# Kernel tuning notes

Measured on AMD Instinct MI355X. Metric: run time of the kernel, lower is better.

The kernel has to match this reference:

```python
import jax, jax.numpy as jnp
import numpy as np

HEADS = 4
DIM_HEAD = 32
EPS = 1e-5

def _layernorm(x, g, b):
    mu = jnp.mean(x, axis=-1, keepdims=True)
    var = jnp.var(x, axis=-1, keepdims=True)
    return (x - mu) * jax.lax.rsqrt(var + EPS) * g + b

def setup_inputs() -> dict:
    key = jax.random.key(0)
    ks = jax.random.split(key, 8)
    B, C, H, W = 16, 256, 32, 32
    N = H * W
    inner = HEADS * DIM_HEAD  # 128
    s = lambda d: 1.0 / np.sqrt(d)
    return {
        "x": jax.random.normal(ks[0], (B, C, H, W), jnp.float32),
        "pos_embedding": jax.random.normal(ks[1], (1, N, C), jnp.float32),
        "w_qkv": jax.random.normal(ks[2], (C, inner * 3), jnp.float32) * s(C),
        "w_out": jax.random.normal(ks[3], (inner, C), jnp.float32) * s(inner),
        "b_out": jnp.zeros((C,), jnp.float32),
        "w_ff1": jax.random.normal(ks[4], (C, inner), jnp.float32) * s(C),
        "b_ff1": jnp.zeros((inner,), jnp.float32),
        "w_ff2": jax.random.normal(ks[5], (inner, C), jnp.float32) * s(inner),
        "b_ff2": jnp.zeros((C,), jnp.float32),
        "g1": jnp.ones((C,), jnp.float32),
        "beta1": jnp.zeros((C,), jnp.float32),
        "g2": jnp.ones((C,), jnp.float32),
        "beta2": jnp.zeros((C,), jnp.float32),
    }

def reference(x, pos_embedding, w_qkv, w_out, b_out, w_ff1, b_ff1, w_ff2, b_ff2, g1, beta1, g2, beta2):
    b, c, h, w = x.shape
    n = h * w
    tok = jnp.transpose(x.reshape(b, c, n), (0, 2, 1))  # [b, n, c]
    tok = tok + pos_embedding  # (dropout is identity at eval)
    # attention
    qkv = _layernorm(tok, g1, beta1) @ w_qkv  # [b, n, 3*inner]
    qkv = qkv.reshape(b, n, 3, HEADS, DIM_HEAD)
    q, k, v = qkv[:, :, 0], qkv[:, :, 1], qkv[:, :, 2]  # [b, n, h, d]
    scale = DIM_HEAD ** -0.5
    dots = jnp.einsum('bihd,bjhd->bhij', q, k) * scale
    attn = jax.nn.softmax(dots, axis=-1)
    out = jnp.einsum('bhij,bjhd->bihd', attn, v).reshape(b, n, HEADS * DIM_HEAD)
    tok = out @ w_out + b_out + tok
    # ffn
    hdn = jax.nn.gelu(_layernorm(tok, g2, beta2) @ w_ff1 + b_ff1, approximate=False)
    tok = hdn @ w_ff2 + b_ff2 + tok
    return jnp.transpose(tok, (0, 2, 1)).reshape(b, c, h, w)
```

## Files before the change

### kernel.cpp

```cpp
#include <hip/hip_runtime.h>
#include <hip/hip_bf16.h>
#include <math.h>

#define B_     16
#define C_     256
#define N_     1024
#define HEADS_ 4
#define DH_    32
#define INNER_ 128
#define EPS_   1e-5f

typedef __attribute__((ext_vector_type(8))) short bf16x8;
typedef __attribute__((ext_vector_type(4))) float f32x4;

__device__ __forceinline__ ushort f2bf(float f) {
  union { float f; unsigned u; } v; v.f = f;
  unsigned u = v.u;
  return (ushort)((u + 0x7fffu + ((u >> 16) & 1u)) >> 16);
}
__device__ __forceinline__ float bf2f(ushort u) {
  union { unsigned u; float f; } v; v.u = ((unsigned)u) << 16;
  return v.f;
}
__device__ __forceinline__ unsigned cvt_pk_bf16(float lo, float hi) {
  unsigned r;
  asm("v_cvt_pk_bf16_f32 %0, %1, %2" : "=v"(r) : "v"(lo), "v"(hi));
  return r;
}

#define QSCALE_ 0.2550348652979437f

__global__ __launch_bounds__(256) void k_wconv(
    const float* __restrict__ wqkv, const float* __restrict__ wout,
    const float* __restrict__ wff1, const float* __restrict__ wff2,
    ushort* __restrict__ wqkvT, ushort* __restrict__ woutT,
    ushort* __restrict__ wff1T, ushort* __restrict__ wff2T) {
  int i = blockIdx.x * 256 + threadIdx.x;
  if (i < 98304) {
    int k = i / 384, n = i % 384;
    wqkvT[n * 256 + k] = f2bf(wqkv[i]);
    return;
  }
  i -= 98304;
  if (i < 32768) {
    int k = i / 256, n = i % 256;
    woutT[n * 128 + k] = f2bf(wout[i]);
    return;
  }
  i -= 32768;
  if (i < 32768) {
    int k = i / 128, n = i % 128;
    wff1T[n * 256 + k] = f2bf(wff1[i]);
    return;
  }
  i -= 32768;
  {
    int k = i / 256, n = i % 256;
    wff2T[n * 128 + k] = f2bf(wff2[i]);
  }
}

union KFusedSmem {
  float  xs[C_][68];
  ushort xnl[64][264];
};

__global__ __launch_bounds__(256) void k_fused(
    const float* __restrict__ x, const float* __restrict__ pos,
    const float* __restrict__ g1, const float* __restrict__ beta1,
    const ushort* __restrict__ wqkvT, ushort* __restrict__ tokb,
    ushort* __restrict__ qb, ushort* __restrict__ kb, ushort* __restrict__ vtb) {
  const int b  = blockIdx.x >> 4;
  const int n0 = (blockIdx.x & 15) << 6;
  const int t  = threadIdx.x;
  __shared__ KFusedSmem u;

  {
    const int cq = t >> 4, nq = t & 15;
#pragma unroll
    for (int i = 0; i < 16; ++i) {
      const int c = i * 16 + cq;
      const float4 v = *reinterpret_cast<const float4*>(
          &x[((size_t)b * C_ + c) * N_ + n0 + 4 * nq]);
      *reinterpret_cast<float4*>(&u.xs[c][4 * nq]) = v;
    }
  }
  __syncthreads();

  {
    const int tl = t >> 2, sub = t & 3, c0 = sub * 64;
    const int n = n0 + tl;
    float v[64];
#pragma unroll
    for (int i = 0; i < 64; ++i) v[i] = u.xs[c0 + i][tl];
#pragma unroll
    for (int j = 0; j < 16; ++j) {
      const float4 p = *reinterpret_cast<const float4*>(&pos[(size_t)n * C_ + c0 + 4 * j]);
      v[4*j] += p.x; v[4*j+1] += p.y; v[4*j+2] += p.z; v[4*j+3] += p.w;
    }
    float s = 0.f;
#pragma unroll
    for (int i = 0; i < 64; ++i) s += v[i];
    s += __shfl_xor(s, 1); s += __shfl_xor(s, 2);
    const float mu = s * (1.f / C_);
    float sq = 0.f;
#pragma unroll
    for (int i = 0; i < 64; ++i) { const float d = v[i] - mu; sq += d * d; }
    sq += __shfl_xor(sq, 1); sq += __shfl_xor(sq, 2);
    const float rs = rsqrtf(sq * (1.f / C_) + EPS_);

    ushort* tokrow = &tokb[((size_t)b * N_ + n) * C_ + c0];
    ushort xn_local[64];
#pragma unroll
    for (int j = 0; j < 16; ++j) {
      ushort4 tu;
      tu.x = f2bf(v[4*j]);   tu.y = f2bf(v[4*j+1]);
      tu.z = f2bf(v[4*j+2]); tu.w = f2bf(v[4*j+3]);
      *reinterpret_cast<ushort4*>(&tokrow[4 * j]) = tu;
      const float4 g  = *reinterpret_cast<const float4*>(&g1[c0 + 4 * j]);
      const float4 be = *reinterpret_cast<const float4*>(&beta1[c0 + 4 * j]);
      xn_local[4*j]   = f2bf((v[4*j]   - mu) * rs * g.x + be.x);
      xn_local[4*j+1] = f2bf((v[4*j+1] - mu) * rs * g.y + be.y);
      xn_local[4*j+2] = f2bf((v[4*j+2] - mu) * rs * g.z + be.z);
      xn_local[4*j+3] = f2bf((v[4*j+3] - mu) * rs * g.w + be.w);
    }
    __syncthreads();
#pragma unroll
    for (int j = 0; j < 16; ++j)
      *reinterpret_cast<ushort4*>(&u.xnl[tl][c0 + 4 * j]) =
          *reinterpret_cast<ushort4*>(&xn_local[4 * j]);
  }
  __syncthreads();

  {
    const int w = t >> 6, lane = t & 63;
    const int li = lane & 15, g = lane >> 4;
#pragma unroll
    for (int mf = 0; mf < 6; ++mf) {
      const int chb = w * 96 + mf * 16;
      bf16x8 Af[8];
#pragma unroll
      for (int ks = 0; ks < 8; ++ks)
        Af[ks] = *reinterpret_cast<const bf16x8*>(
            &wqkvT[(size_t)(chb + li) * C_ + ks * 32 + 8 * g]);
#pragma unroll
      for (int nf = 0; nf < 4; ++nf) {
        bf16x8 Bf[8];
#pragma unroll
        for (int ks = 0; ks < 8; ++ks)
          Bf[ks] = *reinterpret_cast<const bf16x8*>(&u.xnl[nf * 16 + li][ks * 32 + 8 * g]);
        f32x4 acc = {0.f, 0.f, 0.f, 0.f};
#pragma unroll
        for (int ks = 0; ks < 8; ++ks)
          acc = __builtin_amdgcn_mfma_f32_16x16x32_bf16(Af[ks], Bf[ks], acc, 0, 0, 0);
        const int nn = n0 + nf * 16 + li;
        const int ch0 = chb + 4 * g;
        if (ch0 < 128) {
          const int h = ch0 >> 5, dh = ch0 & 31;
          ushort4 uq;
          uq.x = f2bf(acc[0] * QSCALE_); uq.y = f2bf(acc[1] * QSCALE_);
          uq.z = f2bf(acc[2] * QSCALE_); uq.w = f2bf(acc[3] * QSCALE_);
          *reinterpret_cast<ushort4*>(&qb[(((size_t)(b * HEADS_ + h)) * N_ + nn) * DH_ + dh]) = uq;
        } else if (ch0 < 256) {
          const int c2 = ch0 - 128, h = c2 >> 5, dh = c2 & 31;
          ushort4 uk;
          uk.x = f2bf(acc[0]); uk.y = f2bf(acc[1]); uk.z = f2bf(acc[2]); uk.w = f2bf(acc[3]);
          *reinterpret_cast<ushort4*>(&kb[(((size_t)(b * HEADS_ + h)) * N_ + nn) * DH_ + dh]) = uk;
        } else {
          const int c2 = ch0 - 256, h = c2 >> 5, dh = c2 & 31;
          ushort* base = &vtb[(((size_t)(b * HEADS_ + h)) * DH_ + dh) * N_ + nn];
          base[0] = f2bf(acc[0]); base[N_] = f2bf(acc[1]);
          base[2 * N_] = f2bf(acc[2]); base[3 * N_] = f2bf(acc[3]);
        }
      }
    }
  }
}

__global__ __launch_bounds__(256) void k_attn(
    const ushort* __restrict__ qb, const ushort* __restrict__ kb,
    const ushort* __restrict__ vtb, ushort* __restrict__ ao) {
  const int blk = blockIdx.x;
  const int b   = blk >> 5;
  const int h   = (blk >> 3) & 3;
  const int qt2 = blk & 7;
  const int tid = threadIdx.x;
  const int w = tid >> 6, lane = tid & 63;
  const int qi = lane & 15, g = lane >> 4;

  __shared__ __align__(16) ushort P_lds[4][2][16][80];

  const int bh  = b * HEADS_ + h;
  const int nq0 = qt2 * 128 + w * 32;
  const ushort* Kb = kb  + (size_t)bh * N_ * DH_;
  const ushort* Vt = vtb + (size_t)bh * DH_ * N_;

  bf16x8 qf[2];
#pragma unroll
  for (int G = 0; G < 2; ++G)
    qf[G] = *reinterpret_cast<const bf16x8*>(
        qb + ((size_t)bh * N_ + nq0 + G * 16 + qi) * DH_ + 8 * g);

  f32x4 acc[2][2];
#pragma unroll
  for (int G = 0; G < 2; ++G)
#pragma unroll
    for (int d = 0; d < 2; ++d)
#pragma unroll
      for (int r = 0; r < 4; ++r) acc[G][d][r] = 0.f;
  float m[2] = {-INFINITY, -INFINITY};
  float l[2] = {0.f, 0.f};

  for (int jt = 0; jt < 16; ++jt) {
    const int k0 = jt * 64;
    bf16x8 kf[4];
#pragma unroll
    for (int kt = 0; kt < 4; ++kt)
      kf[kt] = *reinterpret_cast<const bf16x8*>(
          Kb + (size_t)(k0 + kt * 16 + qi) * DH_ + 8 * g);
    bf16x8 vf[2][2];
#pragma unroll
    for (int c = 0; c < 2; ++c)
#pragma unroll
      for (int d = 0; d < 2; ++d)
        vf[c][d] = *reinterpret_cast<const bf16x8*>(
            Vt + (size_t)(d * 16 + qi) * N_ + k0 + c * 32 + 8 * g);

    f32x4 s[2][4];
#pragma unroll
    for (int G = 0; G < 2; ++G)
#pragma unroll
      for (int kt = 0; kt < 4; ++kt) {
        f32x4 z = {0.f, 0.f, 0.f, 0.f};
        s[G][kt] = __builtin_amdgcn_mfma_f32_16x16x32_bf16(kf[kt], qf[G], z, 0, 0, 0);
      }

#pragma unroll
    for (int G = 0; G < 2; ++G) {
      float t0 = fmaxf(fmaxf(s[G][0][0], s[G][0][1]), fmaxf(s[G][0][2], s[G][0][3]));
      float t1 = fmaxf(fmaxf(s[G][1][0], s[G][1][1]), fmaxf(s[G][1][2], s[G][1][3]));
      float t2 = fmaxf(fmaxf(s[G][2][0], s[G][2][1]), fmaxf(s[G][2][2], s[G][2][3]));
      float t3 = fmaxf(fmaxf(s[G][3][0], s[G][3][1]), fmaxf(s[G][3][2], s[G][3][3]));
      float tmax = fmaxf(fmaxf(t0, t1), fmaxf(t2, t3));
      tmax = fmaxf(tmax, __shfl_xor(tmax, 16));
      tmax = fmaxf(tmax, __shfl_xor(tmax, 32));
      if (!__all(tmax <= m[G] + 8.0f)) {
        const float nm = fmaxf(m[G], tmax);
        const float corr = exp2f(m[G] - nm);
#pragma unroll
        for (int d = 0; d < 2; ++d)
#pragma unroll
          for (int r = 0; r < 4; ++r) acc[G][d][r] *= corr;
        l[G] *= corr;
        m[G] = nm;
      }
      float psum = 0.f;
#pragma unroll
      for (int kt = 0; kt < 4; ++kt) {
        const float p0 = exp2f(s[G][kt][0] - m[G]);
        const float p1 = exp2f(s[G][kt][1] - m[G]);
        const float p2 = exp2f(s[G][kt][2] - m[G]);
        const float p3 = exp2f(s[G][kt][3] - m[G]);
        psum += (p0 + p1) + (p2 + p3);
        uint2 dw;
        dw.x = cvt_pk_bf16(p0, p1);
        dw.y = cvt_pk_bf16(p2, p3);
        *reinterpret_cast<uint2*>(&P_lds[w][G][qi][kt * 16 + 4 * g]) = dw;
      }
      l[G] += psum;
    }

#pragma unroll
    for (int c = 0; c < 2; ++c) {
      const bf16x8 pf0 = *reinterpret_cast<const bf16x8*>(&P_lds[w][0][qi][c * 32 + 8 * g]);
      const bf16x8 pf1 = *reinterpret_cast<const bf16x8*>(&P_lds[w][1][qi][c * 32 + 8 * g]);
#pragma unroll
      for (int d = 0; d < 2; ++d) {
        acc[0][d] = __builtin_amdgcn_mfma_f32_16x16x32_bf16(vf[c][d], pf0, acc[0][d], 0, 0, 0);
        acc[1][d] = __builtin_amdgcn_mfma_f32_16x16x32_bf16(vf[c][d], pf1, acc[1][d], 0, 0, 0);
      }
    }
  }

#pragma unroll
  for (int G = 0; G < 2; ++G) {
    float lg = l[G];
    lg += __shfl_xor(lg, 16);
    lg += __shfl_xor(lg, 32);
    const float inv = 1.f / lg;
    const int n = nq0 + G * 16 + qi;
#pragma unroll
    for (int d = 0; d < 2; ++d) {
      ushort4 uo;
      uo.x = f2bf(acc[G][d][0] * inv);
      uo.y = f2bf(acc[G][d][1] * inv);
      uo.z = f2bf(acc[G][d][2] * inv);
      uo.w = f2bf(acc[G][d][3] * inv);
      *reinterpret_cast<ushort4*>(
          &ao[((size_t)b * N_ + n) * INNER_ + h * DH_ + d * 16 + 4 * g]) = uo;
    }
  }
}

__global__ __launch_bounds__(256) void k_mlp(
    const ushort* __restrict__ ao, const ushort* __restrict__ tokb,
    const ushort* __restrict__ woutT, const float* __restrict__ b_out,
    const ushort* __restrict__ wff1T, const float* __restrict__ b_ff1,
    const ushort* __restrict__ wff2T, const float* __restrict__ b_ff2,
    const float* __restrict__ g2, const float* __restrict__ beta2,
    float* __restrict__ out) {
  const int T0 = blockIdx.x * 32;
  const int bb = T0 >> 10;
  const int nb = T0 & 1023;
  const int tid = threadIdx.x;
  const int w = tid >> 6, lane = tid & 63, li = lane & 15, g = lane >> 4;

  __shared__ float  t2s[32][260];
  __shared__ ushort xn2[32][264];
  __shared__ ushort hsb[32][136];

  {
    bf16x8 Af[2][4];
#pragma unroll
    for (int mf = 0; mf < 2; ++mf)
#pragma unroll
      for (int ks = 0; ks < 4; ++ks)
        Af[mf][ks] = *reinterpret_cast<const bf16x8*>(
            &ao[((size_t)(T0 + mf * 16 + li)) * INNER_ + ks * 32 + 8 * g]);
#pragma unroll
    for (int nf = 0; nf < 4; ++nf) {
      const int n = w * 64 + nf * 16;
      bf16x8 Bf[4];
#pragma unroll
      for (int ks = 0; ks < 4; ++ks)
        Bf[ks] = *reinterpret_cast<const bf16x8*>(
            &woutT[(size_t)(n + li) * INNER_ + ks * 32 + 8 * g]);
#pragma unroll
      for (int mf = 0; mf < 2; ++mf) {
        f32x4 acc = {0.f, 0.f, 0.f, 0.f};
#pragma unroll
        for (int ks = 0; ks < 4; ++ks)
          acc = __builtin_amdgcn_mfma_f32_16x16x32_bf16(Af[mf][ks], Bf[ks], acc, 0, 0, 0);
        const int nch = n + li;
        const int tl0 = mf * 16 + 4 * g;
        const float bo = b_out[nch];
#pragma unroll
        for (int r = 0; r < 4; ++r)
          t2s[tl0 + r][nch] =
              acc[r] + bo + bf2f(tokb[((size_t)(T0 + tl0 + r)) * C_ + nch]);
      }
    }
  }
  __syncthreads();

  {
    const int tl = tid >> 3, c0 = (tid & 7) * 32;
    float v[32];
#pragma unroll
    for (int j = 0; j < 8; ++j) {
      const float4 t4 = *reinterpret_cast<const float4*>(&t2s[tl][c0 + 4 * j]);
      v[4*j] = t4.x; v[4*j+1] = t4.y; v[4*j+2] = t4.z; v[4*j+3] = t4.w;
    }
    float s = 0.f;
#pragma unroll
    for (int i = 0; i < 32; ++i) s += v[i];
    s += __shfl_xor(s, 1); s += __shfl_xor(s, 2); s += __shfl_xor(s, 4);
    const float mu = s * (1.f / C_);
    float sq = 0.f;
#pragma unroll
    for (int i = 0; i < 32; ++i) { const float d = v[i] - mu; sq += d * d; }
    sq += __shfl_xor(sq, 1); sq += __shfl_xor(sq, 2); sq += __shfl_xor(sq, 4);
    const float rs = rsqrtf(sq * (1.f / C_) + EPS_);
#pragma unroll
    for (int j = 0; j < 8; ++j) {
      const float4 gg = *reinterpret_cast<const float4*>(&g2[c0 + 4 * j]);
      const float4 be = *reinterpret_cast<const float4*>(&beta2[c0 + 4 * j]);
      ushort4 u;
      u.x = f2bf((v[4*j]   - mu) * rs * gg.x + be.x);
      u.y = f2bf((v[4*j+1] - mu) * rs * gg.y + be.y);
      u.z = f2bf((v[4*j+2] - mu) * rs * gg.z + be.z);
      u.w = f2bf((v[4*j+3] - mu) * rs * gg.w + be.w);
      *reinterpret_cast<ushort4*>(&xn2[tl][c0 + 4 * j]) = u;
    }
  }
  __syncthreads();

  {
    bf16x8 Af[2][8];
#pragma unroll
    for (int mf = 0; mf < 2; ++mf)
#pragma unroll
      for (int ks = 0; ks < 8; ++ks)
        Af[mf][ks] = *reinterpret_cast<const bf16x8*>(&xn2[mf * 16 + li][ks * 32 + 8 * g]);
#pragma unroll
    for (int nf = 0; nf < 2; ++nf) {
      const int n = w * 32 + nf * 16;
      bf16x8 Bf[8];
#pragma unroll
      for (int ks = 0; ks < 8; ++ks)
        Bf[ks] = *reinterpret_cast<const bf16x8*>(
            &wff1T[(size_t)(n + li) * C_ + ks * 32 + 8 * g]);
#pragma unroll
      for (int mf = 0; mf < 2; ++mf) {
        f32x4 acc = {0.f, 0.f, 0.f, 0.f};
#pragma unroll
        for (int ks = 0; ks < 8; ++ks)
          acc = __builtin_amdgcn_mfma_f32_16x16x32_bf16(Af[mf][ks], Bf[ks], acc, 0, 0, 0);
        const int nch = n + li;
        const int tl0 = mf * 16 + 4 * g;
        const float bf1 = b_ff1[nch];
#pragma unroll
        for (int r = 0; r < 4; ++r) {
          float hv = acc[r] + bf1;
          hv = 0.5f * hv * (1.f + erff(hv * 0.70710678118654752f));
          hsb[tl0 + r][nch] = f2bf(hv);
        }
      }
    }
  }
  __syncthreads();

  {
    bf16x8 Af[2][4];
#pragma unroll
    for (int mf = 0; mf < 2; ++mf)
#pragma unroll
      for (int ks = 0; ks < 4; ++ks)
        Af[mf][ks] = *reinterpret_cast<const bf16x8*>(&hsb[mf * 16 + li][ks * 32 + 8 * g]);
#pragma unroll
    for (int nf = 0; nf < 4; ++nf) {
      const int n = w * 64 + nf * 16;
      bf16x8 Bf[4];
#pragma unroll
      for (int ks = 0; ks < 4; ++ks)
        Bf[ks] = *reinterpret_cast<const bf16x8*>(
            &wff2T[(size_t)(n + li) * INNER_ + ks * 32 + 8 * g]);
#pragma unroll
      for (int mf = 0; mf < 2; ++mf) {
        f32x4 acc = {0.f, 0.f, 0.f, 0.f};
#pragma unroll
        for (int ks = 0; ks < 4; ++ks)
          acc = __builtin_amdgcn_mfma_f32_16x16x32_bf16(Af[mf][ks], Bf[ks], acc, 0, 0, 0);
        const int nch = n + li;
        const int tl0 = mf * 16 + 4 * g;
        const float bo = b_ff2[nch];
        float4 o;
        o.x = acc[0] + bo + t2s[tl0 + 0][nch];
        o.y = acc[1] + bo + t2s[tl0 + 1][nch];
        o.z = acc[2] + bo + t2s[tl0 + 2][nch];
        o.w = acc[3] + bo + t2s[tl0 + 3][nch];
        *reinterpret_cast<float4*>(
            &out[((size_t)bb * C_ + nch) * N_ + nb + tl0]) = o;
      }
    }
  }
}

extern "C" void kernel_launch(void* const* d_in, const int* in_sizes, int n_in,
                              void* d_out, int out_size, void* d_ws, size_t ws_size,
                              hipStream_t stream) {
  const float* x     = (const float*)d_in[0];
  const float* pos   = (const float*)d_in[1];
  const float* w_qkv = (const float*)d_in[2];
  const float* w_out = (const float*)d_in[3];
  const float* b_out = (const float*)d_in[4];
  const float* w_ff1 = (const float*)d_in[5];
  const float* b_ff1 = (const float*)d_in[6];
  const float* w_ff2 = (const float*)d_in[7];
  const float* b_ff2 = (const float*)d_in[8];
  const float* g1    = (const float*)d_in[9];
  const float* beta1 = (const float*)d_in[10];
  const float* g2    = (const float*)d_in[11];
  const float* beta2 = (const float*)d_in[12];
  float* out = (float*)d_out;

  ushort* tokb  = (ushort*)d_ws;
  ushort* ao    = tokb + 4194304;
  ushort* qb    = ao + 2097152;
  ushort* kb    = qb + 2097152;
  ushort* vtb   = kb + 2097152;
  ushort* wqkvT = vtb + 2097152;
  ushort* woutT = wqkvT + 98304;
  ushort* wff1T = woutT + 32768;
  ushort* wff2T = wff1T + 32768;

  k_wconv<<<768, 256, 0, stream>>>(w_qkv, w_out, w_ff1, w_ff2,
                                   wqkvT, woutT, wff1T, wff2T);
  k_fused<<<256, 256, 0, stream>>>(x, pos, g1, beta1, wqkvT, tokb, qb, kb, vtb);
  k_attn<<<512, 256, 0, stream>>>(qb, kb, vtb, ao);
  k_mlp<<<512, 256, 0, stream>>>(ao, tokb, woutT, b_out, wff1T, b_ff1,
                                 wff2T, b_ff2, g2, beta2, out);
}
```

Baseline: 167.4 us.

## Double k_fused block size and prefetch next K/V tile in attention loop

k_fused now launches 512 threads per block, so each thread handles half as many channels in the layernorm stage and half as many output fragments in the QKV GEMM. This adds parallelism inside the 256-block grid. The attention kernel now loads the next K and V fragments into registers before computing the current tile, hiding global-load latency behind the MFMA and softmax work. The price is higher register pressure in attention and an extra shuffle step in the layernorm reduction.

Result: no change. 165.3 us (-1.3%).

```diff
diff --git a/kernel.cpp b/kernel.cpp
--- a/kernel.cpp
+++ b/kernel.cpp
@@ -65,7 +65,7 @@
   ushort xnl[64][264];
 };
 
-__global__ __launch_bounds__(256) void k_fused(
+__global__ __launch_bounds__(512) void k_fused(
     const float* __restrict__ x, const float* __restrict__ pos,
     const float* __restrict__ g1, const float* __restrict__ beta1,
     const ushort* __restrict__ wqkvT, ushort* __restrict__ tokb,
@@ -76,10 +76,10 @@
   __shared__ KFusedSmem u;
 
   {
-    const int cq = t >> 4, nq = t & 15;
-#pragma unroll
-    for (int i = 0; i < 16; ++i) {
-      const int c = i * 16 + cq;
+    const int nq = t & 15, cq = t >> 4;
+#pragma unroll
+    for (int i = 0; i < 8; ++i) {
+      const int c = i * 32 + cq;
       const float4 v = *reinterpret_cast<const float4*>(
           &x[((size_t)b * C_ + c) * N_ + n0 + 4 * nq]);
       *reinterpret_cast<float4*>(&u.xs[c][4 * nq]) = v;
@@ -88,31 +88,31 @@
   __syncthreads();
 
   {
-    const int tl = t >> 2, sub = t & 3, c0 = sub * 64;
+    const int tl = t >> 3, sub = t & 7, c0 = sub * 32;
     const int n = n0 + tl;
-    float v[64];
-#pragma unroll
-    for (int i = 0; i < 64; ++i) v[i] = u.xs[c0 + i][tl];
-#pragma unroll
-    for (int j = 0; j < 16; ++j) {
+    float v[32];
+#pragma unroll
+    for (int i = 0; i < 32; ++i) v[i] = u.xs[c0 + i][tl];
+#pragma unroll
+    for (int j = 0; j < 8; ++j) {
       const float4 p = *reinterpret_cast<const float4*>(&pos[(size_t)n * C_ + c0 + 4 * j]);
       v[4*j] += p.x; v[4*j+1] += p.y; v[4*j+2] += p.z; v[4*j+3] += p.w;
     }
     float s = 0.f;
 #pragma unroll
-    for (int i = 0; i < 64; ++i) s += v[i];
-    s += __shfl_xor(s, 1); s += __shfl_xor(s, 2);
+    for (int i = 0; i < 32; ++i) s += v[i];
+    s += __shfl_xor(s, 1); s += __shfl_xor(s, 2); s += __shfl_xor(s, 4);
     const float mu = s * (1.f / C_);
     float sq = 0.f;
 #pragma unroll
-    for (int i = 0; i < 64; ++i) { const float d = v[i] - mu; sq += d * d; }
-    sq += __shfl_xor(sq, 1); sq += __shfl_xor(sq, 2);
+    for (int i = 0; i < 32; ++i) { const float d = v[i] - mu; sq += d * d; }
+    sq += __shfl_xor(sq, 1); sq += __shfl_xor(sq, 2); sq += __shfl_xor(sq, 4);
     const float rs = rsqrtf(sq * (1.f / C_) + EPS_);
 
     ushort* tokrow = &tokb[((size_t)b * N_ + n) * C_ + c0];
-    ushort xn_local[64];
-#pragma unroll
-    for (int j = 0; j < 16; ++j) {
+    ushort xn_local[32];
+#pragma unroll
+    for (int j = 0; j < 8; ++j) {
       ushort4 tu;
       tu.x = f2bf(v[4*j]);   tu.y = f2bf(v[4*j+1]);
       tu.z = f2bf(v[4*j+2]); tu.w = f2bf(v[4*j+3]);
@@ -126,7 +126,7 @@
     }
     __syncthreads();
 #pragma unroll
-    for (int j = 0; j < 16; ++j)
+    for (int j = 0; j < 8; ++j)
       *reinterpret_cast<ushort4*>(&u.xnl[tl][c0 + 4 * j]) =
           *reinterpret_cast<ushort4*>(&xn_local[4 * j]);
   }
@@ -136,8 +136,8 @@
     const int w = t >> 6, lane = t & 63;
     const int li = lane & 15, g = lane >> 4;
 #pragma unroll
-    for (int mf = 0; mf < 6; ++mf) {
-      const int chb = w * 96 + mf * 16;
+    for (int mf = 0; mf < 3; ++mf) {
+      const int chb = w * 48 + mf * 16;
       bf16x8 Af[8];
 #pragma unroll
       for (int ks = 0; ks < 8; ++ks)
@@ -211,20 +211,31 @@
   float m[2] = {-INFINITY, -INFINITY};
   float l[2] = {0.f, 0.f};
 
+  bf16x8 kf[4], vf[2][2];
+#pragma unroll
+  for (int kt = 0; kt < 4; ++kt)
+    kf[kt] = *reinterpret_cast<const bf16x8*>(
+        Kb + (size_t)(kt * 16 + qi) * DH_ + 8 * g);
+#pragma unroll
+  for (int c = 0; c < 2; ++c)
+#pragma unroll
+    for (int d = 0; d < 2; ++d)
+      vf[c][d] = *reinterpret_cast<const bf16x8*>(
+          Vt + (size_t)(d * 16 + qi) * N_ + c * 32 + 8 * g);
+
   for (int jt = 0; jt < 16; ++jt) {
-    const int k0 = jt * 64;
-    bf16x8 kf[4];
+    const int kn = (jt < 15 ? jt + 1 : 15) * 64;
+    bf16x8 kfn[4], vfn[2][2];
 #pragma unroll
     for (int kt = 0; kt < 4; ++kt)
-      kf[kt] = *reinterpret_cast<const bf16x8*>(
-          Kb + (size_t)(k0 + kt * 16 + qi) * DH_ + 8 * g);
-    bf16x8 vf[2][2];
+      kfn[kt] = *reinterpret_cast<const bf16x8*>(
+          Kb + (size_t)(kn + kt * 16 + qi) * DH_ + 8 * g);
 #pragma unroll
     for (int c = 0; c < 2; ++c)
 #pragma unroll
       for (int d = 0; d < 2; ++d)
-        vf[c][d] = *reinterpret_cast<const bf16x8*>(
-            Vt + (size_t)(d * 16 + qi) * N_ + k0 + c * 32 + 8 * g);
+        vfn[c][d] = *reinterpret_cast<const bf16x8*>(
+            Vt + (size_t)(d * 16 + qi) * N_ + kn + c * 32 + 8 * g);
 
     f32x4 s[2][4];
 #pragma unroll
@@ -280,6 +291,13 @@
         acc[1][d] = __builtin_amdgcn_mfma_f32_16x16x32_bf16(vf[c][d], pf1, acc[1][d], 0, 0, 0);
       }
     }
+
+#pragma unroll
+    for (int kt = 0; kt < 4; ++kt) kf[kt] = kfn[kt];
+#pragma unroll
+    for (int c = 0; c < 2; ++c)
+#pragma unroll
+      for (int d = 0; d < 2; ++d) vf[c][d] = vfn[c][d];
   }
 
 #pragma unroll
@@ -486,7 +504,7 @@
 
   k_wconv<<<768, 256, 0, stream>>>(w_qkv, w_out, w_ff1, w_ff2,
                                    wqkvT, woutT, wff1T, wff2T);
-  k_fused<<<256, 256, 0, stream>>>(x, pos, g1, beta1, wqkvT, tokb, qb, kb, vtb);
+  k_fused<<<256, 512, 0, stream>>>(x, pos, g1, beta1, wqkvT, tokb, qb, kb, vtb);
   k_attn<<<512, 256, 0, stream>>>(qb, kb, vtb, ao);
   k_mlp<<<512, 256, 0, stream>>>(ao, tokb, woutT, b_out, wff1T, b_ff1,
                                  wff2T, b_ff2, g2, beta2, out);
```
